# Optimization experiments

Measured on AMD Instinct MI355X. Metric: run time of the kernel, lower is better.

The kernel has to match this reference:

```python
import jax, jax.numpy as jnp
import numpy as np

NEG_RATIO = 3.0           # negative_ratio
FALLBACK_NEG = 0.0        # fallback_negative_num
EPS = 1e-6                # eps
LOG_CLAMP = -100.0        # torch BCELoss clamps log to -100


def setup_inputs() -> dict:
    key = jax.random.key(0)
    k1, k2, k3 = jax.random.split(key, 3)
    shape = (32, 640, 640)  # [B, H, W] DBNet-style shrink maps
    # probabilities strictly inside (0,1)
    pred = jax.random.uniform(k1, shape, jnp.float32, 1e-4, 1.0 - 1e-4)
    gt = (jax.random.uniform(k2, shape) < 0.05).astype(jnp.float32)
    mask = (jax.random.uniform(k3, shape) < 0.9).astype(jnp.float32)
    return {"pred": pred, "gt": gt, "mask": mask}


def reference(pred, gt, mask):
    positive = gt * mask
    negative = (1.0 - gt) * mask
    # torch uses int(sum()); masks are binary so sums are integral, floor is exact
    pos_count = jnp.floor(positive.sum())
    neg_total = jnp.floor(negative.sum())
    neg_count = jnp.where(
        pos_count == 0,
        jnp.minimum(neg_total, FALLBACK_NEG),
        jnp.minimum(neg_total, jnp.floor(pos_count * NEG_RATIO)),
    )

    # BCE with torch's log clamp at -100
    log_p = jnp.maximum(jnp.log(pred), LOG_CLAMP)
    log_1mp = jnp.maximum(jnp.log1p(-pred), LOG_CLAMP)
    loss = -(gt * log_p + (1.0 - gt) * log_1mp)

    positive_sum = (loss * positive).sum()

    # hard-negative mining: take the top `neg_count` negative losses.
    # neg_count is data-dependent, so sort descending and mask by rank
    # (jit-compatible, same math as torch.topk(...).sum()).
    neg_loss = (loss * negative).reshape(-1)
    neg_sorted = -jnp.sort(-neg_loss)  # descending
    ranks = jnp.arange(neg_sorted.shape[0], dtype=jnp.float32)
    negative_sum = jnp.where(ranks < neg_count, neg_sorted, 0.0).sum()

    return (positive_sum + negative_sum) / (pos_count + neg_count + EPS)
```

## Files before the change

kernel.cpp:

```cpp
#include <hip/hip_runtime.h>
#include <math.h>


#define NBINS1 4096
#define K1_BLOCKS 2048

struct Ctrl {
  unsigned long long pos_cnt;
  unsigned long long neg_cnt;
  unsigned long long k;
  double pos_sum;
  unsigned B;
  unsigned k_rem;
};

#define LN2F 0.69314718055994530942f

__device__ __forceinline__ double bin_mid(unsigned b) {
  return (double)__uint_as_float((b << 19) | 0x40000u);
}

__device__ __forceinline__ void proc1(float p, float g, float m,
                                      unsigned& pc, unsigned& nc,
                                      double& psum, unsigned* __restrict__ hc) {
  bool gpos = (g != 0.0f);
  bool valid = (m != 0.0f);
  bool ispos = valid && gpos;
  bool isneg = valid && !gpos;
  float x = gpos ? p : 1.0f - p;
  float loss = -fmaxf(__log2f(x) * LN2F, -100.0f);
  pc += ispos ? 1u : 0u;
  nc += isneg ? 1u : 0u;
  psum += ispos ? (double)loss : 0.0;
  if (isneg) atomicAdd(&hc[__float_as_uint(loss) >> 19], 1u);
}

extern "C" __global__ void __launch_bounds__(256, 8)
k1_hist(const float* __restrict__ pred, const float* __restrict__ gt,
        const float* __restrict__ mask, unsigned* __restrict__ hist1,
        Ctrl* __restrict__ ctrl, int n4, int n) {
  __shared__ unsigned h[NBINS1];
  for (int i = threadIdx.x; i < NBINS1; i += blockDim.x) h[i] = 0u;
  __syncthreads();

  int wv = threadIdx.x >> 6, ln = threadIdx.x & 63;

  unsigned pc = 0, nc = 0;
  double psum = 0.0;
  const float4* p4 = (const float4*)pred;
  const float4* g4 = (const float4*)gt;
  const float4* m4 = (const float4*)mask;
  int gtid = blockIdx.x * blockDim.x + threadIdx.x;
  int S = gridDim.x * blockDim.x;

  int i = gtid;
  for (; i + 3 * S < n4; i += 4 * S) {
    float4 pv0 = p4[i];
    float4 pv1 = p4[i + S];
    float4 pv2 = p4[i + 2 * S];
    float4 pv3 = p4[i + 3 * S];
    float4 gv0 = g4[i];
    float4 gv1 = g4[i + S];
    float4 gv2 = g4[i + 2 * S];
    float4 gv3 = g4[i + 3 * S];
    float4 mv0 = m4[i];
    float4 mv1 = m4[i + S];
    float4 mv2 = m4[i + 2 * S];
    float4 mv3 = m4[i + 3 * S];

    proc1(pv0.x, gv0.x, mv0.x, pc, nc, psum, h);
    proc1(pv0.y, gv0.y, mv0.y, pc, nc, psum, h);
    proc1(pv0.z, gv0.z, mv0.z, pc, nc, psum, h);
    proc1(pv0.w, gv0.w, mv0.w, pc, nc, psum, h);
    proc1(pv1.x, gv1.x, mv1.x, pc, nc, psum, h);
    proc1(pv1.y, gv1.y, mv1.y, pc, nc, psum, h);
    proc1(pv1.z, gv1.z, mv1.z, pc, nc, psum, h);
    proc1(pv1.w, gv1.w, mv1.w, pc, nc, psum, h);
    proc1(pv2.x, gv2.x, mv2.x, pc, nc, psum, h);
    proc1(pv2.y, gv2.y, mv2.y, pc, nc, psum, h);
    proc1(pv2.z, gv2.z, mv2.z, pc, nc, psum, h);
    proc1(pv2.w, gv2.w, mv2.w, pc, nc, psum, h);
    proc1(pv3.x, gv3.x, mv3.x, pc, nc, psum, h);
    proc1(pv3.y, gv3.y, mv3.y, pc, nc, psum, h);
    proc1(pv3.z, gv3.z, mv3.z, pc, nc, psum, h);
    proc1(pv3.w, gv3.w, mv3.w, pc, nc, psum, h);
  }
  for (; i < n4; i += S) {
    float4 pv = p4[i], gv = g4[i], mv = m4[i];
    proc1(pv.x, gv.x, mv.x, pc, nc, psum, h);
    proc1(pv.y, gv.y, mv.y, pc, nc, psum, h);
    proc1(pv.z, gv.z, mv.z, pc, nc, psum, h);
    proc1(pv.w, gv.w, mv.w, pc, nc, psum, h);
  }
  for (int t = n4 * 4 + gtid; t < n; t += S) {
    proc1(pred[t], gt[t], mask[t], pc, nc, psum, h);
  }

  unsigned long long pcl = pc, ncl = nc;
  for (int off = 32; off > 0; off >>= 1) {
    pcl += __shfl_down(pcl, off);
    ncl += __shfl_down(ncl, off);
    psum += __shfl_down(psum, off);
  }
  __shared__ unsigned long long spc[4], snc[4];
  __shared__ double sps[4];
  if (ln == 0) { spc[wv] = pcl; snc[wv] = ncl; sps[wv] = psum; }
  __syncthreads();
  if (threadIdx.x == 0) {
    unsigned long long tp = 0, tn = 0; double ts = 0.0;
    for (int w = 0; w < 4; w++) { tp += spc[w]; tn += snc[w]; ts += sps[w]; }
    atomicAdd(&ctrl->pos_cnt, tp);
    atomicAdd(&ctrl->neg_cnt, tn);
    unsafeAtomicAdd(&ctrl->pos_sum, ts);
  }
  for (int b = threadIdx.x; b < NBINS1; b += blockDim.x) {
    unsigned c = h[b];
    if (c) atomicAdd(&hist1[b], c);
  }
}

extern "C" __global__ void __launch_bounds__(256)
k5_final(const unsigned* __restrict__ hist1, Ctrl* __restrict__ ctrl,
         float* __restrict__ out) {
  const int T = 256, CH = NBINS1 / T;
  __shared__ unsigned long long sarr[T];
  __shared__ unsigned long long sk;
  __shared__ unsigned sB, skrem;
  __shared__ double sred[4];
  int t = threadIdx.x;
  int wv = t >> 6, ln = t & 63;

  unsigned cnt[CH];
  unsigned long long tot = 0;
  for (int j = 0; j < CH; j++) { cnt[j] = hist1[t * CH + j]; tot += cnt[j]; }
  sarr[t] = tot;
  if (t == 0) {
    sB = 0xFFFFFFFFu; skrem = 0u;
    unsigned long long pos = ctrl->pos_cnt, negtot = ctrl->neg_cnt;
    unsigned long long k = 0;
    if (pos > 0) {
      k = pos * 3ull;
      if (k > negtot) k = negtot;
    }
    ctrl->k = k;
    sk = k;
  }
  __syncthreads();
  for (int off = 1; off < T; off <<= 1) {
    unsigned long long v = (t + off < T) ? sarr[t + off] : 0ull;
    __syncthreads();
    sarr[t] += v;
    __syncthreads();
  }
  unsigned long long k = sk;
  if (k > 0) {
    unsigned long long above = sarr[t] - tot;
    if (above < k && sarr[t] >= k) {
      unsigned long long cum = above;
      for (int j = CH - 1; j >= 0; j--) {
        if (cum + (unsigned long long)cnt[j] >= k) {
          sB = (unsigned)(t * CH + j);
          skrem = (unsigned)(k - cum);
          break;
        }
        cum += cnt[j];
      }
    }
  }
  __syncthreads();
  unsigned B = sB;

  double s = 0.0;
  if (B != 0xFFFFFFFFu) {
    for (int j = 0; j < CH; j++) {
      unsigned bi = (unsigned)(t * CH + j);
      if (bi > B && cnt[j]) s += (double)cnt[j] * bin_mid(bi);
    }
  }
  for (int off = 32; off > 0; off >>= 1) s += __shfl_down(s, off);
  if (ln == 0) sred[wv] = s;
  __syncthreads();
  if (t == 0) {
    double neg_sum = sred[0] + sred[1] + sred[2] + sred[3];
    if (skrem > 0 && B != 0xFFFFFFFFu)
      neg_sum += (double)skrem * bin_mid(B);
    double denom = (double)ctrl->pos_cnt + (double)k + 1e-6;
    out[0] = (float)((ctrl->pos_sum + neg_sum) / denom);
  }
}

extern "C" void kernel_launch(void* const* d_in, const int* in_sizes, int n_in,
                              void* d_out, int out_size, void* d_ws, size_t ws_size,
                              hipStream_t stream) {
  const float* pred = (const float*)d_in[0];
  const float* gt   = (const float*)d_in[1];
  const float* mask = (const float*)d_in[2];
  float* out = (float*)d_out;
  int n = in_sizes[0];
  int n4 = n / 4;
  char* ws = (char*)d_ws;

  const size_t HIST1_OFF = 256;
  const size_t ZERO_BYTES = HIST1_OFF + NBINS1 * sizeof(unsigned);

  Ctrl* ctrl = (Ctrl*)ws;
  unsigned* hist1 = (unsigned*)(ws + HIST1_OFF);

  hipMemsetAsync(d_ws, 0, ZERO_BYTES, stream);
  k1_hist<<<K1_BLOCKS, 256, 0, stream>>>(pred, gt, mask, hist1, ctrl, n4, n);
  k5_final<<<1, 256, 0, stream>>>(hist1, ctrl, out);
}
```

Measured before the change: 224.0 us.

## Pipeline input streaming through LDS with async global_load_lds triple buffering

Replaces the register-unrolled grid-stride loads with a three-deep software pipeline that uses global_load_lds to stream pred/gt/mask tiles straight into per-wave LDS buffers, gated by explicit vmcnt waits. The grid shrinks to 768 blocks and launch bounds drop to 3 blocks per SM to make room for the extra LDS. The aim is to keep more memory requests in flight while the log/histogram work runs, hiding latency in this bandwidth-bound pass. It relies on hand-counted vmcnt values and per-wave LDS reuse without barriers, and lower occupancy could cost latency hiding if the pipeline depth is not enough.

```diff
diff --git a/kernel.cpp b/kernel.cpp
--- a/kernel.cpp
+++ b/kernel.cpp
@@ -3,7 +3,8 @@
 
 
 #define NBINS1 4096
-#define K1_BLOCKS 2048
+#define K1_BLOCKS 768
+#define DEPTH 3
 
 struct Ctrl {
   unsigned long long pos_cnt;
@@ -35,11 +36,35 @@
   if (isneg) atomicAdd(&hc[__float_as_uint(loss) >> 19], 1u);
 }
 
-extern "C" __global__ void __launch_bounds__(256, 8)
+__device__ __forceinline__ void stage3(const float4* __restrict__ p4,
+                                       const float4* __restrict__ g4,
+                                       const float4* __restrict__ m4,
+                                       int idx, float4* sl) {
+  typedef const __attribute__((address_space(1))) void gvoid_t;
+  typedef __attribute__((address_space(3))) void lvoid_t;
+  __builtin_amdgcn_global_load_lds((gvoid_t*)(p4 + idx), (lvoid_t*)(sl + 0 * 64), 16, 0, 0);
+  __builtin_amdgcn_global_load_lds((gvoid_t*)(g4 + idx), (lvoid_t*)(sl + 1 * 64), 16, 0, 0);
+  __builtin_amdgcn_global_load_lds((gvoid_t*)(m4 + idx), (lvoid_t*)(sl + 2 * 64), 16, 0, 0);
+}
+
+__device__ __forceinline__ void proc_buf(const float4* sl, int ln,
+                                         unsigned& pc, unsigned& nc,
+                                         double& psum, unsigned* __restrict__ h) {
+  float4 pv = sl[0 * 64 + ln];
+  float4 gv = sl[1 * 64 + ln];
+  float4 mv = sl[2 * 64 + ln];
+  proc1(pv.x, gv.x, mv.x, pc, nc, psum, h);
+  proc1(pv.y, gv.y, mv.y, pc, nc, psum, h);
+  proc1(pv.z, gv.z, mv.z, pc, nc, psum, h);
+  proc1(pv.w, gv.w, mv.w, pc, nc, psum, h);
+}
+
+extern "C" __global__ void __launch_bounds__(256, 3)
 k1_hist(const float* __restrict__ pred, const float* __restrict__ gt,
         const float* __restrict__ mask, unsigned* __restrict__ hist1,
         Ctrl* __restrict__ ctrl, int n4, int n) {
   __shared__ unsigned h[NBINS1];
+  __shared__ float4 sbuf[DEPTH][4][3 * 64];
   for (int i = threadIdx.x; i < NBINS1; i += blockDim.x) h[i] = 0u;
   __syncthreads();
 
@@ -53,39 +78,37 @@
   int gtid = blockIdx.x * blockDim.x + threadIdx.x;
   int S = gridDim.x * blockDim.x;
 
-  int i = gtid;
-  for (; i + 3 * S < n4; i += 4 * S) {
-    float4 pv0 = p4[i];
-    float4 pv1 = p4[i + S];
-    float4 pv2 = p4[i + 2 * S];
-    float4 pv3 = p4[i + 3 * S];
-    float4 gv0 = g4[i];
-    float4 gv1 = g4[i + S];
-    float4 gv2 = g4[i + 2 * S];
-    float4 gv3 = g4[i + 3 * S];
-    float4 mv0 = m4[i];
-    float4 mv1 = m4[i + S];
-    float4 mv2 = m4[i + 2 * S];
-    float4 mv3 = m4[i + 3 * S];
-
-    proc1(pv0.x, gv0.x, mv0.x, pc, nc, psum, h);
-    proc1(pv0.y, gv0.y, mv0.y, pc, nc, psum, h);
-    proc1(pv0.z, gv0.z, mv0.z, pc, nc, psum, h);
-    proc1(pv0.w, gv0.w, mv0.w, pc, nc, psum, h);
-    proc1(pv1.x, gv1.x, mv1.x, pc, nc, psum, h);
-    proc1(pv1.y, gv1.y, mv1.y, pc, nc, psum, h);
-    proc1(pv1.z, gv1.z, mv1.z, pc, nc, psum, h);
-    proc1(pv1.w, gv1.w, mv1.w, pc, nc, psum, h);
-    proc1(pv2.x, gv2.x, mv2.x, pc, nc, psum, h);
-    proc1(pv2.y, gv2.y, mv2.y, pc, nc, psum, h);
-    proc1(pv2.z, gv2.z, mv2.z, pc, nc, psum, h);
-    proc1(pv2.w, gv2.w, mv2.w, pc, nc, psum, h);
-    proc1(pv3.x, gv3.x, mv3.x, pc, nc, psum, h);
-    proc1(pv3.y, gv3.y, mv3.y, pc, nc, psum, h);
-    proc1(pv3.z, gv3.z, mv3.z, pc, nc, psum, h);
-    proc1(pv3.w, gv3.w, mv3.w, pc, nc, psum, h);
-  }
-  for (; i < n4; i += S) {
+  int FULL = n4 / S;
+  int PST = (FULL >= DEPTH) ? FULL : 0;
+
+  if (PST) {
+    stage3(p4, g4, m4, 0 * S + gtid, &sbuf[0][wv][0]);
+    stage3(p4, g4, m4, 1 * S + gtid, &sbuf[1][wv][0]);
+    stage3(p4, g4, m4, 2 * S + gtid, &sbuf[2][wv][0]);
+    int buf = 0;
+    for (int it = 0; it < PST - DEPTH; ++it) {
+      float4* sl = &sbuf[buf][wv][0];
+      asm volatile("s_waitcnt vmcnt(6)" ::: "memory");
+      __builtin_amdgcn_sched_barrier(0);
+      proc_buf(sl, ln, pc, nc, psum, h);
+      __builtin_amdgcn_sched_barrier(0);
+      stage3(p4, g4, m4, (it + DEPTH) * S + gtid, sl);
+      buf = (buf == DEPTH - 1) ? 0 : buf + 1;
+    }
+    asm volatile("s_waitcnt vmcnt(6)" ::: "memory");
+    __builtin_amdgcn_sched_barrier(0);
+    proc_buf(&sbuf[buf][wv][0], ln, pc, nc, psum, h);
+    buf = (buf == DEPTH - 1) ? 0 : buf + 1;
+    asm volatile("s_waitcnt vmcnt(3)" ::: "memory");
+    __builtin_amdgcn_sched_barrier(0);
+    proc_buf(&sbuf[buf][wv][0], ln, pc, nc, psum, h);
+    buf = (buf == DEPTH - 1) ? 0 : buf + 1;
+    asm volatile("s_waitcnt vmcnt(0)" ::: "memory");
+    __builtin_amdgcn_sched_barrier(0);
+    proc_buf(&sbuf[buf][wv][0], ln, pc, nc, psum, h);
+  }
+
+  for (int i = PST * S + gtid; i < n4; i += S) {
     float4 pv = p4[i], gv = g4[i], mv = m4[i];
     proc1(pv.x, gv.x, mv.x, pc, nc, psum, h);
     proc1(pv.y, gv.y, mv.y, pc, nc, psum, h);
```

New measurement: 191.0 us. 1.17x faster.

## Fuse memset, histogram and finalize into one cooperative kernel with grid syncs

Applied to the files above, without the earlier changes.

Replaces the memset plus two kernel launches with a single cooperative kernel. It zeroes the workspace, builds the histogram, grid-syncs, and then block 0 does the top-k selection and final division. The grid is reduced from 2048 to 1024 blocks, capped by occupancy, and launch bounds drop to 4 blocks per CU. This removes launch and memset overhead, but adds two grid-wide barriers and fewer resident waves, which may reduce memory-latency hiding.

```diff
diff --git a/kernel.cpp b/kernel.cpp
--- a/kernel.cpp
+++ b/kernel.cpp
@@ -1,9 +1,10 @@
 #include <hip/hip_runtime.h>
+#include <hip/hip_cooperative_groups.h>
 #include <math.h>
 
 
 #define NBINS1 4096
-#define K1_BLOCKS 2048
+#define K1_BLOCKS 1024
 
 struct Ctrl {
   unsigned long long pos_cnt;
@@ -35,13 +36,25 @@
   if (isneg) atomicAdd(&hc[__float_as_uint(loss) >> 19], 1u);
 }
 
-extern "C" __global__ void __launch_bounds__(256, 8)
-k1_hist(const float* __restrict__ pred, const float* __restrict__ gt,
-        const float* __restrict__ mask, unsigned* __restrict__ hist1,
-        Ctrl* __restrict__ ctrl, int n4, int n) {
+extern "C" __global__ void __launch_bounds__(256, 4)
+mega(const float* __restrict__ pred, const float* __restrict__ gt,
+     const float* __restrict__ mask, unsigned* __restrict__ hist1,
+     Ctrl* __restrict__ ctrl, float* __restrict__ out, int n4, int n) {
+  cooperative_groups::grid_group gg = cooperative_groups::this_grid();
+
+  int gtid = blockIdx.x * blockDim.x + threadIdx.x;
+  int S = gridDim.x * blockDim.x;
+
+  for (int i = gtid; i < NBINS1; i += S) hist1[i] = 0u;
+  if (gtid == 0) {
+    ctrl->pos_cnt = 0ull; ctrl->neg_cnt = 0ull; ctrl->k = 0ull;
+    ctrl->pos_sum = 0.0; ctrl->B = 0u; ctrl->k_rem = 0u;
+  }
+
   __shared__ unsigned h[NBINS1];
   for (int i = threadIdx.x; i < NBINS1; i += blockDim.x) h[i] = 0u;
-  __syncthreads();
+
+  gg.sync();
 
   int wv = threadIdx.x >> 6, ln = threadIdx.x & 63;
 
@@ -50,8 +63,6 @@
   const float4* p4 = (const float4*)pred;
   const float4* g4 = (const float4*)gt;
   const float4* m4 = (const float4*)mask;
-  int gtid = blockIdx.x * blockDim.x + threadIdx.x;
-  int S = gridDim.x * blockDim.x;
 
   int i = gtid;
   for (; i + 3 * S < n4; i += 4 * S) {
@@ -117,6 +128,170 @@
     unsigned c = h[b];
     if (c) atomicAdd(&hist1[b], c);
   }
+
+  __threadfence();
+  gg.sync();
+
+  if (blockIdx.x != 0) return;
+  {
+    const int T = 256, CH = NBINS1 / T;
+    __shared__ unsigned long long sarr[T];
+    __shared__ unsigned long long sk;
+    __shared__ unsigned sB, skrem;
+    __shared__ double sred[4];
+    int t = threadIdx.x;
+
+    unsigned cnt[CH];
+    unsigned long long tot = 0;
+    for (int j = 0; j < CH; j++) {
+      cnt[j] = __hip_atomic_load(&hist1[t * CH + j], __ATOMIC_RELAXED,
+                                 __HIP_MEMORY_SCOPE_AGENT);
+      tot += cnt[j];
+    }
+    sarr[t] = tot;
+    if (t == 0) {
+      sB = 0xFFFFFFFFu; skrem = 0u;
+      unsigned long long pos = __hip_atomic_load(&ctrl->pos_cnt, __ATOMIC_RELAXED,
+                                                 __HIP_MEMORY_SCOPE_AGENT);
+      unsigned long long negtot = __hip_atomic_load(&ctrl->neg_cnt, __ATOMIC_RELAXED,
+                                                    __HIP_MEMORY_SCOPE_AGENT);
+      unsigned long long k = 0;
+      if (pos > 0) {
+        k = pos * 3ull;
+        if (k > negtot) k = negtot;
+      }
+      ctrl->k = k;
+      sk = k;
+    }
+    __syncthreads();
+    for (int off = 1; off < T; off <<= 1) {
+      unsigned long long v = (t + off < T) ? sarr[t + off] : 0ull;
+      __syncthreads();
+      sarr[t] += v;
+      __syncthreads();
+    }
+    unsigned long long k = sk;
+    if (k > 0) {
+      unsigned long long above = sarr[t] - tot;
+      if (above < k && sarr[t] >= k) {
+        unsigned long long cum = above;
+        for (int j = CH - 1; j >= 0; j--) {
+          if (cum + (unsigned long long)cnt[j] >= k) {
+            sB = (unsigned)(t * CH + j);
+            skrem = (unsigned)(k - cum);
+            break;
+          }
+          cum += cnt[j];
+        }
+      }
+    }
+    __syncthreads();
+    unsigned B = sB;
+
+    double s = 0.0;
+    if (B != 0xFFFFFFFFu) {
+      for (int j = 0; j < CH; j++) {
+        unsigned bi = (unsigned)(t * CH + j);
+        if (bi > B && cnt[j]) s += (double)cnt[j] * bin_mid(bi);
+      }
+    }
+    for (int off = 32; off > 0; off >>= 1) s += __shfl_down(s, off);
+    if (ln == 0) sred[wv] = s;
+    __syncthreads();
+    if (t == 0) {
+      double neg_sum = sred[0] + sred[1] + sred[2] + sred[3];
+      if (skrem > 0 && B != 0xFFFFFFFFu)
+        neg_sum += (double)skrem * bin_mid(B);
+      double pos_sum = __hip_atomic_load(&ctrl->pos_sum, __ATOMIC_RELAXED,
+                                         __HIP_MEMORY_SCOPE_AGENT);
+      double posd = (double)__hip_atomic_load(&ctrl->pos_cnt, __ATOMIC_RELAXED,
+                                              __HIP_MEMORY_SCOPE_AGENT);
+      double denom = posd + (double)k + 1e-6;
+      out[0] = (float)((pos_sum + neg_sum) / denom);
+    }
+  }
+}
+
+extern "C" __global__ void __launch_bounds__(256, 4)
+k1_hist(const float* __restrict__ pred, const float* __restrict__ gt,
+        const float* __restrict__ mask, unsigned* __restrict__ hist1,
+        Ctrl* __restrict__ ctrl, int n4, int n) {
+  __shared__ unsigned h[NBINS1];
+  for (int i = threadIdx.x; i < NBINS1; i += blockDim.x) h[i] = 0u;
+  __syncthreads();
+
+  int wv = threadIdx.x >> 6, ln = threadIdx.x & 63;
+  unsigned pc = 0, nc = 0;
+  double psum = 0.0;
+  const float4* p4 = (const float4*)pred;
+  const float4* g4 = (const float4*)gt;
+  const float4* m4 = (const float4*)mask;
+  int gtid = blockIdx.x * blockDim.x + threadIdx.x;
+  int S = gridDim.x * blockDim.x;
+
+  int i = gtid;
+  for (; i + 3 * S < n4; i += 4 * S) {
+    float4 pv0 = p4[i];
+    float4 pv1 = p4[i + S];
+    float4 pv2 = p4[i + 2 * S];
+    float4 pv3 = p4[i + 3 * S];
+    float4 gv0 = g4[i];
+    float4 gv1 = g4[i + S];
+    float4 gv2 = g4[i + 2 * S];
+    float4 gv3 = g4[i + 3 * S];
+    float4 mv0 = m4[i];
+    float4 mv1 = m4[i + S];
+    float4 mv2 = m4[i + 2 * S];
+    float4 mv3 = m4[i + 3 * S];
+    proc1(pv0.x, gv0.x, mv0.x, pc, nc, psum, h);
+    proc1(pv0.y, gv0.y, mv0.y, pc, nc, psum, h);
+    proc1(pv0.z, gv0.z, mv0.z, pc, nc, psum, h);
+    proc1(pv0.w, gv0.w, mv0.w, pc, nc, psum, h);
+    proc1(pv1.x, gv1.x, mv1.x, pc, nc, psum, h);
+    proc1(pv1.y, gv1.y, mv1.y, pc, nc, psum, h);
+    proc1(pv1.z, gv1.z, mv1.z, pc, nc, psum, h);
+    proc1(pv1.w, gv1.w, mv1.w, pc, nc, psum, h);
+    proc1(pv2.x, gv2.x, mv2.x, pc, nc, psum, h);
+    proc1(pv2.y, gv2.y, mv2.y, pc, nc, psum, h);
+    proc1(pv2.z, gv2.z, mv2.z, pc, nc, psum, h);
+    proc1(pv2.w, gv2.w, mv2.w, pc, nc, psum, h);
+    proc1(pv3.x, gv3.x, mv3.x, pc, nc, psum, h);
+    proc1(pv3.y, gv3.y, mv3.y, pc, nc, psum, h);
+    proc1(pv3.z, gv3.z, mv3.z, pc, nc, psum, h);
+    proc1(pv3.w, gv3.w, mv3.w, pc, nc, psum, h);
+  }
+  for (; i < n4; i += S) {
+    float4 pv = p4[i], gv = g4[i], mv = m4[i];
+    proc1(pv.x, gv.x, mv.x, pc, nc, psum, h);
+    proc1(pv.y, gv.y, mv.y, pc, nc, psum, h);
+    proc1(pv.z, gv.z, mv.z, pc, nc, psum, h);
+    proc1(pv.w, gv.w, mv.w, pc, nc, psum, h);
+  }
+  for (int t = n4 * 4 + gtid; t < n; t += S) {
+    proc1(pred[t], gt[t], mask[t], pc, nc, psum, h);
+  }
+
+  unsigned long long pcl = pc, ncl = nc;
+  for (int off = 32; off > 0; off >>= 1) {
+    pcl += __shfl_down(pcl, off);
+    ncl += __shfl_down(ncl, off);
+    psum += __shfl_down(psum, off);
+  }
+  __shared__ unsigned long long spc[4], snc[4];
+  __shared__ double sps[4];
+  if (ln == 0) { spc[wv] = pcl; snc[wv] = ncl; sps[wv] = psum; }
+  __syncthreads();
+  if (threadIdx.x == 0) {
+    unsigned long long tp = 0, tn = 0; double ts = 0.0;
+    for (int w = 0; w < 4; w++) { tp += spc[w]; tn += snc[w]; ts += sps[w]; }
+    atomicAdd(&ctrl->pos_cnt, tp);
+    atomicAdd(&ctrl->neg_cnt, tn);
+    unsafeAtomicAdd(&ctrl->pos_sum, ts);
+  }
+  for (int b = threadIdx.x; b < NBINS1; b += blockDim.x) {
+    unsigned c = h[b];
+    if (c) atomicAdd(&hist1[b], c);
+  }
 }
 
 extern "C" __global__ void __launch_bounds__(256)
@@ -201,11 +376,32 @@
   char* ws = (char*)d_ws;
 
   const size_t HIST1_OFF = 256;
-  const size_t ZERO_BYTES = HIST1_OFF + NBINS1 * sizeof(unsigned);
-
   Ctrl* ctrl = (Ctrl*)ws;
   unsigned* hist1 = (unsigned*)(ws + HIST1_OFF);
 
+  static int coop_blocks = -1;
+  if (coop_blocks < 0) {
+    int nb = 0;
+    hipError_t oe = hipOccupancyMaxActiveBlocksPerMultiprocessor(
+        &nb, (const void*)mega, 256, 0);
+    if (oe == hipSuccess && nb >= 1) {
+      int cap = nb * 256;
+      coop_blocks = (cap < K1_BLOCKS) ? cap : K1_BLOCKS;
+    } else {
+      coop_blocks = 0;
+    }
+  }
+
+  if (coop_blocks > 0) {
+    void* args[] = {(void*)&pred, (void*)&gt, (void*)&mask, (void*)&hist1,
+                    (void*)&ctrl, (void*)&out, (void*)&n4, (void*)&n};
+    hipError_t e = hipLaunchCooperativeKernel(
+        (const void*)mega, dim3(coop_blocks), dim3(256), args, 0, stream);
+    if (e == hipSuccess) return;
+    coop_blocks = 0;
+  }
+
+  const size_t ZERO_BYTES = HIST1_OFF + NBINS1 * sizeof(unsigned);
   hipMemsetAsync(d_ws, 0, ZERO_BYTES, stream);
   k1_hist<<<K1_BLOCKS, 256, 0, stream>>>(pred, gt, mask, hist1, ctrl, n4, n);
   k5_final<<<1, 256, 0, stream>>>(hist1, ctrl, out);
```

Result: slower. 407.9 us (+82.1%).
